# Optimization experiments

Hardware: AMD Instinct MI355X
Metric: run time of the kernel (lower is better)

## Reference

```python
import jax, jax.numpy as jnp
import numpy as np

B, S, D = 1, 8192, 1024
H, HD = 16, 64
WIN = 1024      # sliding_window_size
CHUNK = 1024    # chunk_size
OVERLAP = 128   # chunk_overlap


def setup_inputs() -> dict:
    key = jax.random.key(0)
    ks = jax.random.split(key, 5)
    s = 1.0 / np.sqrt(D)
    inp = {"x": jax.random.normal(ks[0], (B, S, D), jnp.float32)}
    for i, n in enumerate(["Wq", "Wk", "Wv", "Wo"]):
        inp[n] = jax.random.normal(ks[1 + i], (D, D), jnp.float32) * s
    for n in ["bq", "bk", "bv", "bo"]:
        inp[n] = jnp.zeros((D,), jnp.float32)
    return inp


def _attend_chunk(q, k, v, chunk_start, win_start):
    # q: [B, Lq, H, HD]; k, v: [B, Lk, H, HD]
    Lq, Lk = q.shape[1], k.shape[1]
    q_abs = chunk_start + jnp.arange(Lq)[:, None]   # absolute query positions
    k_abs = win_start + jnp.arange(Lk)[None, :]     # absolute key positions
    allowed = (k_abs >= q_abs - WIN // 2) & (k_abs < q_abs + WIN // 2)
    scale = 1.0 / np.sqrt(HD)
    scores = jnp.einsum('bqhd,bkhd->bhqk', q, k) * scale  # [B,H,Lq,Lk]
    scores = jnp.where(allowed[None, None], scores, -jnp.inf)
    p = jax.nn.softmax(scores, axis=-1)
    return jnp.einsum('bhqk,bkhd->bqhd', p, v)


def _overlap_weight(cs, ce):
    # replicate torch linspace overlap-add blend weights (host-side constants)
    w = np.ones(ce - cs, np.float32)
    if cs > 0:
        n = min(cs + OVERLAP, ce) - cs
        w[:n] = np.linspace(0.0, 1.0, n, dtype=np.float32)
    if ce < S:
        os_ = max(cs, ce - OVERLAP)
        w[os_ - cs:] = np.linspace(1.0, 0.0, ce - os_, dtype=np.float32)
    return jnp.asarray(w)


def reference(x, Wq, bq, Wk, bk, Wv, bv, Wo, bo):
    q = (x @ Wq.T + bq).reshape(B, S, H, HD)
    k = (x @ Wk.T + bk).reshape(B, S, H, HD)
    v = (x @ Wv.T + bv).reshape(B, S, H, HD)
    out = jnp.zeros((B, S, H, HD), x.dtype)
    step = CHUNK - OVERLAP
    for cs in range(0, S, step):  # static Python loop over ~10 chunks
        ce = min(cs + CHUNK, S)
        ws, we = max(0, cs - WIN // 2), min(S, ce + WIN // 2)
        o = _attend_chunk(q[:, cs:ce], k[:, ws:we], v[:, ws:we], cs, ws)
        w = _overlap_weight(cs, ce)
        out = out.at[:, cs:ce].add(o * w[None, :, None, None])
    out = out.reshape(B, S, D)
    return out @ Wo.T + bo
```

## Files before the change

### kernel.cpp

```cpp
#include <hip/hip_runtime.h>

#define DEVI __device__ __forceinline__

constexpr int S = 8192, D = 1024, H = 16, HD = 64;
constexpr int NQKV = 3 * D;

typedef __attribute__((ext_vector_type(8))) __bf16 bf16x8;
typedef __attribute__((ext_vector_type(4))) __bf16 bf16x4;
typedef __attribute__((ext_vector_type(8))) unsigned short us8;
typedef __attribute__((ext_vector_type(4))) float f32x4;

DEVI unsigned short f2b(float f) {
  unsigned int u = __float_as_uint(f);
  u += 0x7fff + ((u >> 16) & 1);
  return (unsigned short)(u >> 16);
}

DEVI ushort4 cvt4(float4 v) {
  ushort4 r; r.x = f2b(v.x); r.y = f2b(v.y); r.z = f2b(v.z); r.w = f2b(v.w); return r;
}

DEVI void load_lds16b(const void* g, void* l) {
  __builtin_amdgcn_global_load_lds((const __attribute__((address_space(1))) void*)g,
                                   (__attribute__((address_space(3))) void*)l,
                                   16, 0, 0);
}

__global__ void prep_kernel(const float4* __restrict__ x,
                            const float4* __restrict__ Wq, const float4* __restrict__ Wk,
                            const float4* __restrict__ Wv, const float4* __restrict__ Wo,
                            const float4* __restrict__ bq, const float4* __restrict__ bk,
                            const float4* __restrict__ bv,
                            ushort4* __restrict__ xb, ushort4* __restrict__ wqkv,
                            ushort4* __restrict__ wob, float4* __restrict__ biasq)
{
  constexpr int NX = S * D / 4;
  constexpr int NW = D * D / 4;
  constexpr int NB = D / 4;
  constexpr int TOT = NX + 4 * NW + 3 * NB;
  for (int i = blockIdx.x * blockDim.x + threadIdx.x; i < TOT; i += gridDim.x * blockDim.x) {
    if (i < NX) {
      xb[i] = cvt4(x[i]);
    } else if (i < NX + 3 * NW) {
      int j = i - NX;
      const float4* src = (j < NW) ? Wq : ((j < 2 * NW) ? Wk : Wv);
      int jj = (j < NW) ? j : ((j < 2 * NW) ? j - NW : j - 2 * NW);
      wqkv[j] = cvt4(src[jj]);
    } else if (i < NX + 4 * NW) {
      int j = i - NX - 3 * NW;
      wob[j] = cvt4(Wo[j]);
    } else {
      int j = i - NX - 4 * NW;
      const float4* src = (j < NB) ? bq : ((j < 2 * NB) ? bk : bv);
      int jj = (j < NB) ? j : ((j < 2 * NB) ? j - NB : j - 2 * NB);
      biasq[j] = src[jj];
    }
  }
}

template<int LDC, bool OUT_BF16>
__global__ __launch_bounds__(256)
void gemm_nt(const unsigned short* __restrict__ A,
             const unsigned short* __restrict__ B,
             const float* __restrict__ bias,
             void* __restrict__ C, int K)
{
  __shared__ __align__(16) unsigned short As[128 * 32];
  __shared__ __align__(16) unsigned short Bs[128 * 32];
  const int tid = threadIdx.x;
  const int wave = tid >> 6, lane = tid & 63;
  const int quad = lane >> 4, l15 = lane & 15;
  const int m0 = blockIdx.x * 128, n0 = blockIdx.y * 128;
  const int wr = wave >> 1, wc = wave & 1;

  const f32x4 fzero = {0.f, 0.f, 0.f, 0.f};
  f32x4 acc[4][4];
#pragma unroll
  for (int i = 0; i < 4; ++i)
#pragma unroll
    for (int j = 0; j < 4; ++j) acc[i][j] = fzero;

  const int segr = lane >> 2;
  const int cpst = lane & 3;

  for (int k0 = 0; k0 < K; k0 += 32) {
    __syncthreads();
#pragma unroll
    for (int j = 0; j < 4; ++j) {
      const int s = wave * 4 + j;
      const int s7 = s & 7;
      const int r = s7 * 16 + segr;
      const int c = cpst ^ ((r >> 1) & 3);
      const unsigned short* g = (s < 8)
        ? A + (size_t)(m0 + r) * K + k0 + c * 8
        : B + (size_t)(n0 + r) * K + k0 + c * 8;
      unsigned short* l = ((s < 8) ? As : Bs) + s7 * 512;
      load_lds16b(g, l);
    }
    __syncthreads();

    bf16x8 af[4], bfr[4];
#pragma unroll
    for (int it = 0; it < 4; ++it) {
      const int r = wr * 64 + it * 16 + l15;
      const int cp = quad ^ ((r >> 1) & 3);
      af[it] = *(const bf16x8*)&As[r * 32 + cp * 8];
    }
#pragma unroll
    for (int jt = 0; jt < 4; ++jt) {
      const int r = wc * 64 + jt * 16 + l15;
      const int cp = quad ^ ((r >> 1) & 3);
      bfr[jt] = *(const bf16x8*)&Bs[r * 32 + cp * 8];
    }
#pragma unroll
    for (int it = 0; it < 4; ++it)
#pragma unroll
      for (int jt = 0; jt < 4; ++jt)
        acc[it][jt] = __builtin_amdgcn_mfma_f32_16x16x32_bf16(af[it], bfr[jt], acc[it][jt], 0, 0, 0);
  }

#pragma unroll
  for (int it = 0; it < 4; ++it)
#pragma unroll
    for (int jt = 0; jt < 4; ++jt) {
      const int col = n0 + wc * 64 + jt * 16 + l15;
      const float bv = bias[col];
#pragma unroll
      for (int i = 0; i < 4; ++i) {
        const int row = m0 + wr * 64 + it * 16 + quad * 4 + i;
        const float v = acc[it][jt][i] + bv;
        if constexpr (OUT_BF16)
          ((unsigned short*)C)[(size_t)row * LDC + col] = f2b(v);
        else
          ((float*)C)[(size_t)row * LDC + col] = v;
      }
    }
}

__global__ __launch_bounds__(256)
void attn_fused(const unsigned short* __restrict__ qkv,
                unsigned short* __restrict__ attnb)
{
  __shared__ __align__(16) unsigned short Vt[2][64 * 72];
  __shared__ __align__(16) unsigned short Ps[4][16 * 40];
  const int tid = threadIdx.x;
  const int wave = tid >> 6, lane = tid & 63;
  const int quad = lane >> 4, l15 = lane & 15;
  const int h = blockIdx.y;
  const int q0 = blockIdx.x * 128;
  const int wq0 = q0 + wave * 32;

  const unsigned short* Qp = qkv + h * HD;
  const unsigned short* Kp = qkv + D + h * HD;
  const unsigned short* Vp = qkv + 2 * D + h * HD;

  bf16x8 qf[2][2];
#pragma unroll
  for (int rt = 0; rt < 2; ++rt)
#pragma unroll
    for (int ksp = 0; ksp < 2; ++ksp)
      qf[rt][ksp] = *(const bf16x8*)(Qp + (size_t)(wq0 + rt * 16 + l15) * NQKV + ksp * 32 + quad * 8);

  const f32x4 fzero = {0.f, 0.f, 0.f, 0.f};
  f32x4 o[2][4];
  float lr[2] = {0.f, 0.f};
#pragma unroll
  for (int rt = 0; rt < 2; ++rt)
#pragma unroll
    for (int vt = 0; vt < 4; ++vt) o[rt][vt] = fzero;

  const int ks = (q0 >= 512) ? (q0 - 512) : 0;
  const int ke = (q0 + 640 < S) ? (q0 + 640) : S;

  const int skey = tid >> 3;
  const int sg   = tid & 7;

  us8 vreg[2];

#define LOAD_V(kt_)                                                               \
  {                                                                               \
    _Pragma("unroll")                                                             \
    for (int r = 0; r < 2; ++r)                                                   \
      vreg[r] = *(const us8*)(Vp + (size_t)((kt_) + skey + r * 32) * NQKV + sg * 8); \
  }
#define SCAT_V(b_)                                                                \
  {                                                                               \
    _Pragma("unroll")                                                             \
    for (int r = 0; r < 2; ++r) {                                                 \
      const int key = skey + r * 32;                                              \
      const int ch = (key >> 3) ^ sg;                                             \
      unsigned short* dst = &Vt[b_][sg * 8 * 72 + ch * 8 + (key & 7)];            \
      _Pragma("unroll")                                                           \
      for (int j = 0; j < 8; ++j) dst[j * 72] = vreg[r][j];                       \
    }                                                                             \
  }

  LOAD_V(ks);
  SCAT_V(0);

  constexpr float L2E8 = 0.18033688011112042f;

  int b = 0;
  for (int kt = ks; kt < ke; kt += 64, b ^= 1) {
    __syncthreads();
    const int nx = kt + 64;
    const bool more = (nx < ke);
    if (more) LOAD_V(nx);

    if (kt + 63 >= wq0 - 512 && kt <= wq0 + 542) {
      unsigned short* Pw = (unsigned short*)Ps[wave];
#pragma unroll
      for (int st = 0; st < 2; ++st) {
        const int C0 = kt + st * 32;
        if (!((C0 + 31 >= wq0 - 512) && (C0 <= wq0 + 542))) continue;

        bf16x8 kf[2][2];
#pragma unroll
        for (int hh2 = 0; hh2 < 2; ++hh2)
#pragma unroll
          for (int ksp = 0; ksp < 2; ++ksp)
            kf[hh2][ksp] = *(const bf16x8*)(Kp + (size_t)(C0 + hh2 * 16 + l15) * NQKV
                                            + ksp * 32 + quad * 8);
        bf16x8 vf[4];
#pragma unroll
        for (int vt = 0; vt < 4; ++vt) {
          const int d = vt * 16 + l15;
          vf[vt] = *(const bf16x8*)&Vt[b][d * 72 + (((st * 4 + quad) ^ (d >> 3)) & 7) * 8];
        }

#pragma unroll
        for (int rt = 0; rt < 2; ++rt) {
          const int R = wq0 + rt * 16;
          if (!((C0 + 31 >= R - 512) && (C0 <= R + 526))) continue;
          const int qa = R + l15;

#pragma unroll
          for (int hh2 = 0; hh2 < 2; ++hh2) {
            const int C = C0 + hh2 * 16;
            const bool any  = (C + 15 >= R - 512) && (C <= R + 526);
            const bool full = (C >= R - 497) && (C <= R + 496);
            float p[4];
            if (!any) {
              p[0] = p[1] = p[2] = p[3] = 0.f;
            } else {
              f32x4 z = fzero;
              z = __builtin_amdgcn_mfma_f32_16x16x32_bf16(kf[hh2][0], qf[rt][0], z, 0, 0, 0);
              z = __builtin_amdgcn_mfma_f32_16x16x32_bf16(kf[hh2][1], qf[rt][1], z, 0, 0, 0);
              if (full) {
#pragma unroll
                for (int i = 0; i < 4; ++i) p[i] = __builtin_amdgcn_exp2f(z[i] * L2E8);
              } else {
                const int base = C + quad * 4 - qa + 512;
#pragma unroll
                for (int i = 0; i < 4; ++i)
                  p[i] = ((unsigned)(base + i) < 1024u) ? __builtin_amdgcn_exp2f(z[i] * L2E8) : 0.f;
              }
            }
            lr[rt] += p[0] + p[1] + p[2] + p[3];
            f32x4 pv = {p[0], p[1], p[2], p[3]};
            *(bf16x4*)&Pw[l15 * 40 + hh2 * 16 + quad * 4] = __builtin_convertvector(pv, bf16x4);
          }
          const bf16x8 pf = *(const bf16x8*)&Pw[l15 * 40 + quad * 8];
#pragma unroll
          for (int vt = 0; vt < 4; ++vt)
            o[rt][vt] = __builtin_amdgcn_mfma_f32_16x16x32_bf16(pf, vf[vt], o[rt][vt], 0, 0, 0);
        }
      }
    }

    if (more) SCAT_V(b ^ 1);
  }

  float lt[2];
#pragma unroll
  for (int rt = 0; rt < 2; ++rt) {
    float l = lr[rt];
    l += __shfl_xor(l, 16);
    l += __shfl_xor(l, 32);
    lt[rt] = l;
  }
#pragma unroll
  for (int rt = 0; rt < 2; ++rt)
#pragma unroll
    for (int i = 0; i < 4; ++i) {
      const float lq = __shfl(lt[rt], quad * 4 + i);
      const int qa = wq0 + rt * 16 + quad * 4 + i;
      const float w = (qa >= S - 128) ? (1.0f + (float)(qa - (S - 128)) * (1.0f / 127.0f)) : 1.0f;
      const float scl = w / lq;
#pragma unroll
      for (int vt = 0; vt < 4; ++vt)
        ((__bf16*)attnb)[(size_t)qa * D + h * HD + vt * 16 + l15] = (__bf16)(o[rt][vt][i] * scl);
    }
#undef LOAD_V
#undef SCAT_V
}

extern "C" void kernel_launch(void* const* d_in, const int* in_sizes, int n_in,
                              void* d_out, int out_size, void* d_ws, size_t ws_size,
                              hipStream_t stream)
{
  const float* x  = (const float*)d_in[0];
  const float* Wq = (const float*)d_in[1];
  const float* Wk = (const float*)d_in[2];
  const float* Wv = (const float*)d_in[3];
  const float* Wo = (const float*)d_in[4];
  const float* bq = (const float*)d_in[5];
  const float* bk = (const float*)d_in[6];
  const float* bv = (const float*)d_in[7];
  const float* bo = (const float*)d_in[8];

  char* ws = (char*)d_ws;
  unsigned short* xb    = (unsigned short*)(ws);
  unsigned short* wqkv  = (unsigned short*)(ws + 16777216);
  unsigned short* wob   = (unsigned short*)(ws + 23068672);
  float*          biasq = (float*)         (ws + 25165824);
  unsigned short* qkv   = (unsigned short*)(ws + 25178112);
  unsigned short* attnb = (unsigned short*)(ws + 75509760);

  prep_kernel<<<2048, 256, 0, stream>>>((const float4*)x, (const float4*)Wq, (const float4*)Wk,
                                        (const float4*)Wv, (const float4*)Wo, (const float4*)bq,
                                        (const float4*)bk, (const float4*)bv,
                                        (ushort4*)xb, (ushort4*)wqkv, (ushort4*)wob, (float4*)biasq);

  gemm_nt<NQKV, true><<<dim3(64, 24), 256, 0, stream>>>(xb, wqkv, biasq, (void*)qkv, D);
  attn_fused<<<dim3(S / 128, H), 256, 0, stream>>>(qkv, attnb);
  gemm_nt<D, false><<<dim3(64, 8), 256, 0, stream>>>(attnb, wob, bo, d_out, D);
}
```

Measured before the change: 310.8 us.

## Pre-transpose V and stage K/V tiles into LDS via async global_load_lds

Adds a separate kernel that writes a head-major transposed copy of V into the now-free x buffer. The attention kernel then stages both K and V tiles straight into swizzled LDS with global_load_lds, instead of reading K from global memory per wave and scattering V through registers. The QK/softmax phase is split from the PV phase, with P kept per row-tile in LDS, and the two QK MFMAs use independent accumulators. The aim is to cut redundant global K loads and the scalar LDS scatter stores, at the cost of an extra kernel launch, an extra pass over V, and more LDS use.

```diff
diff --git a/kernel.cpp b/kernel.cpp
--- a/kernel.cpp
+++ b/kernel.cpp
@@ -138,11 +138,35 @@
 }
 
 __global__ __launch_bounds__(256)
+void transpose_v(const unsigned short* __restrict__ qkv, unsigned short* __restrict__ vtb)
+{
+  __shared__ unsigned short T[64 * 72];
+  const int tid = threadIdx.x;
+  const int kb = blockIdx.x, h = blockIdx.y;
+  const unsigned short* Vp = qkv + 2 * D + h * HD;
+  const int key = tid >> 3, sg = tid & 7;
+#pragma unroll
+  for (int r = 0; r < 2; ++r) {
+    us8 v = *(const us8*)(Vp + (size_t)(kb * 64 + key + r * 32) * NQKV + sg * 8);
+    unsigned short* dst = &T[sg * 8 * 72 + key + r * 32];
+#pragma unroll
+    for (int j = 0; j < 8; ++j) dst[j * 72] = v[j];
+  }
+  __syncthreads();
+  const int d = tid >> 2, kc = tid & 3;
+  us8* outp = (us8*)(vtb + (size_t)h * HD * S + (size_t)d * S + kb * 64 + kc * 16);
+  outp[0] = *(const us8*)&T[d * 72 + kc * 16];
+  outp[1] = *(const us8*)&T[d * 72 + kc * 16 + 8];
+}
+
+__global__ __launch_bounds__(256)
 void attn_fused(const unsigned short* __restrict__ qkv,
+                const unsigned short* __restrict__ vtb,
                 unsigned short* __restrict__ attnb)
 {
-  __shared__ __align__(16) unsigned short Vt[2][64 * 72];
-  __shared__ __align__(16) unsigned short Ps[4][16 * 40];
+  __shared__ __align__(16) unsigned short Ks[2][64 * 64];
+  __shared__ __align__(16) unsigned short Vt[2][64 * 64];
+  __shared__ __align__(16) unsigned short Ps[4][2][16 * 72];
   const int tid = threadIdx.x;
   const int wave = tid >> 6, lane = tid & 63;
   const int quad = lane >> 4, l15 = lane & 15;
@@ -152,7 +176,7 @@
 
   const unsigned short* Qp = qkv + h * HD;
   const unsigned short* Kp = qkv + D + h * HD;
-  const unsigned short* Vp = qkv + 2 * D + h * HD;
+  const unsigned short* Vh = vtb + (size_t)h * HD * S;
 
   bf16x8 qf[2][2];
 #pragma unroll
@@ -167,75 +191,56 @@
 #pragma unroll
   for (int rt = 0; rt < 2; ++rt)
 #pragma unroll
-    for (int vt = 0; vt < 4; ++vt) o[rt][vt] = fzero;
+    for (int vt2 = 0; vt2 < 4; ++vt2) o[rt][vt2] = fzero;
 
   const int ks = (q0 >= 512) ? (q0 - 512) : 0;
   const int ke = (q0 + 640 < S) ? (q0 + 640) : S;
 
-  const int skey = tid >> 3;
+  const int srow = tid >> 3;
   const int sg   = tid & 7;
-
-  us8 vreg[2];
-
-#define LOAD_V(kt_)                                                               \
-  {                                                                               \
-    _Pragma("unroll")                                                             \
-    for (int r = 0; r < 2; ++r)                                                   \
-      vreg[r] = *(const us8*)(Vp + (size_t)((kt_) + skey + r * 32) * NQKV + sg * 8); \
-  }
-#define SCAT_V(b_)                                                                \
+  const int scol = sg ^ (srow & 7);
+
+#define STAGE(kt_, b_)                                                            \
   {                                                                               \
     _Pragma("unroll")                                                             \
     for (int r = 0; r < 2; ++r) {                                                 \
-      const int key = skey + r * 32;                                              \
-      const int ch = (key >> 3) ^ sg;                                             \
-      unsigned short* dst = &Vt[b_][sg * 8 * 72 + ch * 8 + (key & 7)];            \
-      _Pragma("unroll")                                                           \
-      for (int j = 0; j < 8; ++j) dst[j * 72] = vreg[r][j];                       \
+      load_lds16b(Kp + (size_t)((kt_) + srow + r * 32) * NQKV + scol * 8,         \
+                  &Ks[b_][(size_t)tid * 8 + r * 2048]);                           \
+      load_lds16b(Vh + (size_t)(srow + r * 32) * S + (kt_) + scol * 8,            \
+                  &Vt[b_][(size_t)tid * 8 + r * 2048]);                           \
     }                                                                             \
   }
 
-  LOAD_V(ks);
-  SCAT_V(0);
+  STAGE(ks, 0);
 
   constexpr float L2E8 = 0.18033688011112042f;
 
   int b = 0;
   for (int kt = ks; kt < ke; kt += 64, b ^= 1) {
     __syncthreads();
-    const int nx = kt + 64;
-    const bool more = (nx < ke);
-    if (more) LOAD_V(nx);
+    if (kt + 64 < ke) STAGE(kt + 64, b ^ 1);
 
     if (kt + 63 >= wq0 - 512 && kt <= wq0 + 542) {
-      unsigned short* Pw = (unsigned short*)Ps[wave];
+      bf16x8 kf[4][2];
+#pragma unroll
+      for (int hh = 0; hh < 4; ++hh)
+#pragma unroll
+        for (int ksp = 0; ksp < 2; ++ksp)
+          kf[hh][ksp] = *(const bf16x8*)&Ks[b][(hh * 16 + l15) * 64
+                                              + ((ksp * 4 + quad) ^ (l15 & 7)) * 8];
+
 #pragma unroll
       for (int st = 0; st < 2; ++st) {
         const int C0 = kt + st * 32;
-        if (!((C0 + 31 >= wq0 - 512) && (C0 <= wq0 + 542))) continue;
-
-        bf16x8 kf[2][2];
-#pragma unroll
-        for (int hh2 = 0; hh2 < 2; ++hh2)
-#pragma unroll
-          for (int ksp = 0; ksp < 2; ++ksp)
-            kf[hh2][ksp] = *(const bf16x8*)(Kp + (size_t)(C0 + hh2 * 16 + l15) * NQKV
-                                            + ksp * 32 + quad * 8);
-        bf16x8 vf[4];
-#pragma unroll
-        for (int vt = 0; vt < 4; ++vt) {
-          const int d = vt * 16 + l15;
-          vf[vt] = *(const bf16x8*)&Vt[b][d * 72 + (((st * 4 + quad) ^ (d >> 3)) & 7) * 8];
-        }
-
 #pragma unroll
         for (int rt = 0; rt < 2; ++rt) {
           const int R = wq0 + rt * 16;
           if (!((C0 + 31 >= R - 512) && (C0 <= R + 526))) continue;
           const int qa = R + l15;
-
+          unsigned short* Pw = (unsigned short*)Ps[wave][rt];
 #pragma unroll
           for (int hh2 = 0; hh2 < 2; ++hh2) {
+            const int hh = st * 2 + hh2;
             const int C = C0 + hh2 * 16;
             const bool any  = (C + 15 >= R - 512) && (C <= R + 526);
             const bool full = (C >= R - 497) && (C <= R + 496);
@@ -243,9 +248,10 @@
             if (!any) {
               p[0] = p[1] = p[2] = p[3] = 0.f;
             } else {
-              f32x4 z = fzero;
-              z = __builtin_amdgcn_mfma_f32_16x16x32_bf16(kf[hh2][0], qf[rt][0], z, 0, 0, 0);
-              z = __builtin_amdgcn_mfma_f32_16x16x32_bf16(kf[hh2][1], qf[rt][1], z, 0, 0, 0);
+              f32x4 z0 = fzero, z1 = fzero;
+              z0 = __builtin_amdgcn_mfma_f32_16x16x32_bf16(kf[hh][0], qf[rt][0], z0, 0, 0, 0);
+              z1 = __builtin_amdgcn_mfma_f32_16x16x32_bf16(kf[hh][1], qf[rt][1], z1, 0, 0, 0);
+              const f32x4 z = z0 + z1;
               if (full) {
 #pragma unroll
                 for (int i = 0; i < 4; ++i) p[i] = __builtin_amdgcn_exp2f(z[i] * L2E8);
@@ -258,17 +264,32 @@
             }
             lr[rt] += p[0] + p[1] + p[2] + p[3];
             f32x4 pv = {p[0], p[1], p[2], p[3]};
-            *(bf16x4*)&Pw[l15 * 40 + hh2 * 16 + quad * 4] = __builtin_convertvector(pv, bf16x4);
+            *(bf16x4*)&Pw[l15 * 72 + hh * 16 + quad * 4] = __builtin_convertvector(pv, bf16x4);
           }
-          const bf16x8 pf = *(const bf16x8*)&Pw[l15 * 40 + quad * 8];
-#pragma unroll
-          for (int vt = 0; vt < 4; ++vt)
-            o[rt][vt] = __builtin_amdgcn_mfma_f32_16x16x32_bf16(pf, vf[vt], o[rt][vt], 0, 0, 0);
         }
       }
-    }
-
-    if (more) SCAT_V(b ^ 1);
+
+#pragma unroll
+      for (int st = 0; st < 2; ++st) {
+        const int C0 = kt + st * 32;
+        if (!((C0 + 31 >= wq0 - 512) && (C0 <= wq0 + 542))) continue;
+        bf16x8 vf[4];
+#pragma unroll
+        for (int vt2 = 0; vt2 < 4; ++vt2) {
+          const int d = vt2 * 16 + l15;
+          vf[vt2] = *(const bf16x8*)&Vt[b][d * 64 + (((st * 4 + quad) ^ (d & 7))) * 8];
+        }
+#pragma unroll
+        for (int rt = 0; rt < 2; ++rt) {
+          const int R = wq0 + rt * 16;
+          if (!((C0 + 31 >= R - 512) && (C0 <= R + 526))) continue;
+          const bf16x8 pf = *(const bf16x8*)&Ps[wave][rt][l15 * 72 + (st * 4 + quad) * 8];
+#pragma unroll
+          for (int vt2 = 0; vt2 < 4; ++vt2)
+            o[rt][vt2] = __builtin_amdgcn_mfma_f32_16x16x32_bf16(pf, vf[vt2], o[rt][vt2], 0, 0, 0);
+        }
+      }
+    }
   }
 
   float lt[2];
@@ -288,11 +309,10 @@
       const float w = (qa >= S - 128) ? (1.0f + (float)(qa - (S - 128)) * (1.0f / 127.0f)) : 1.0f;
       const float scl = w / lq;
 #pragma unroll
-      for (int vt = 0; vt < 4; ++vt)
-        ((__bf16*)attnb)[(size_t)qa * D + h * HD + vt * 16 + l15] = (__bf16)(o[rt][vt][i] * scl);
-    }
-#undef LOAD_V
-#undef SCAT_V
+      for (int vt2 = 0; vt2 < 4; ++vt2)
+        ((__bf16*)attnb)[(size_t)qa * D + h * HD + vt2 * 16 + l15] = (__bf16)(o[rt][vt2][i] * scl);
+    }
+#undef STAGE
 }
 
 extern "C" void kernel_launch(void* const* d_in, const int* in_sizes, int n_in,
@@ -316,6 +336,7 @@
   float*          biasq = (float*)         (ws + 25165824);
   unsigned short* qkv   = (unsigned short*)(ws + 25178112);
   unsigned short* attnb = (unsigned short*)(ws + 75509760);
+  unsigned short* vtb   = xb;
 
   prep_kernel<<<2048, 256, 0, stream>>>((const float4*)x, (const float4*)Wq, (const float4*)Wk,
                                         (const float4*)Wv, (const float4*)Wo, (const float4*)bq,
@@ -323,6 +344,7 @@
                                         (ushort4*)xb, (ushort4*)wqkv, (ushort4*)wob, (float4*)biasq);
 
   gemm_nt<NQKV, true><<<dim3(64, 24), 256, 0, stream>>>(xb, wqkv, biasq, (void*)qkv, D);
-  attn_fused<<<dim3(S / 128, H), 256, 0, stream>>>(qkv, attnb);
+  transpose_v<<<dim3(S / 64, H), 256, 0, stream>>>(qkv, vtb);
+  attn_fused<<<dim3(S / 128, H), 256, 0, stream>>>(qkv, vtb, attnb);
   gemm_nt<D, false><<<dim3(64, 8), 256, 0, stream>>>(attnb, wob, bo, d_out, D);
 }
```

Result: faster. 303.6 us (-2.3%).
